# Kernel optimization log

Measured on AMD Instinct MI355X. Metric: run time of the kernel, lower is better.

Reference implementation:

```python
import jax, jax.numpy as jnp
import numpy as np

H, DH, RK, RD = 16, 128, 512, 64  # num_heads, head_dim, kv_lora_rank, rope_dim


def apply_rope(x, cos, sin):
    # x: [..., L, ..., rope_dim]; cos/sin: [L, rope_dim//2]
    cos = cos[None, :, None, :]
    sin = sin[None, :, None, :]
    x1, x2 = x[..., 0::2], x[..., 1::2]
    out_real = x1 * cos - x2 * sin
    out_imag = x1 * sin + x2 * cos
    return jnp.stack([out_real, out_imag], axis=-1).reshape(x.shape)


def setup_inputs() -> dict:
    key = jax.random.key(0)
    ks = jax.random.split(key, 7)
    B, L, E, MAXLEN = 2, 2048, 2048, 4096
    x = jax.random.normal(ks[0], (B, L, E), dtype=jnp.float32)
    cos_table = jax.random.uniform(ks[1], (MAXLEN, RD // 2), dtype=jnp.float32)
    sin_table = jax.random.uniform(ks[2], (MAXLEN, RD // 2), dtype=jnp.float32)
    wq = jax.random.normal(ks[3], (E, H * (DH + RD)), dtype=jnp.float32) / np.sqrt(E)
    wkv_down = jax.random.normal(ks[4], (E, RK + RD), dtype=jnp.float32) / np.sqrt(E)
    w_up = jax.random.normal(ks[5], (RK, H * (2 * DH + RD)), dtype=jnp.float32) / np.sqrt(RK)
    w_out = jax.random.normal(ks[6], (H * (DH + RD), E), dtype=jnp.float32) / np.sqrt(H * (DH + RD))
    return {"x": x, "cos_table": cos_table, "sin_table": sin_table,
            "wq": wq, "wkv_down": wkv_down, "w_up": w_up, "w_out": w_out}


def reference(x, cos_table, sin_table, wq, wkv_down, w_up, w_out):
    # Prefill path (use_cache=False): idx = 0, kv comes from current tokens only.
    B, L, E = x.shape
    cos = cos_table[:L]
    sin = sin_table[:L]

    # Queries: per-head content part + rope part
    q_all = (x @ wq).reshape(B, L, H, DH + RD)
    q_head, q_rope = q_all[..., :DH], q_all[..., DH:]
    q_rope = apply_rope(q_rope, cos, sin)
    q = jnp.concatenate([q_head, q_rope], axis=-1)  # [B,L,H,DH+RD]

    # Compressed KV latent + shared rope key
    kv_lat = x @ wkv_down                            # [B,L,RK+RD]
    c_kv = kv_lat[..., :RK]
    k_rope = kv_lat[..., RK:]
    k_rope = apply_rope(k_rope[:, :, None, :], cos, sin)[:, :, 0, :]  # [B,L,RD]

    # Up-project latent to per-head K/V
    up = (c_kv @ w_up).reshape(B, L, H, 2 * DH + RD)
    k_head = up[..., :DH]
    v_head = up[..., DH:2 * DH]
    v_rope = up[..., 2 * DH:]
    k_rope_b = jnp.broadcast_to(k_rope[:, :, None, :], (B, L, H, RD))
    k = jnp.concatenate([k_head, k_rope_b], axis=-1)  # [B,L,H,DH+RD]
    v = jnp.concatenate([v_head, v_rope], axis=-1)    # [B,L,H,DH+RD]

    # Causal attention (query_indices = arange(L), key_indices = arange(L))
    scale = 1.0 / jnp.sqrt(jnp.float32(DH + RD))
    scores = jnp.einsum('blhd,bshd->bhls', q, k) * scale
    idxs = jnp.arange(L)
    bias = jnp.where(idxs[:, None] >= idxs[None, :], 0.0, -1000000000.0)
    attn = jax.nn.softmax(scores + bias[None, None, :, :], axis=-1)
    out = jnp.einsum('bhls,bshd->blhd', attn, v)  # [B,L,H,DH+RD]
    return out.reshape(B, L, -1) @ w_out
```

## Files before the change

kernel.cpp:

```cpp
#include <hip/hip_runtime.h>
#include <stdint.h>

#define H_ 16
#define DH_ 128
#define RK_ 512
#define RD_ 64
#define B_ 2
#define L_ 2048
#define E_ 2048
#define DQ_ 192
#define NQ_ (H_*DQ_)
#define NKV_ 576
#define NKVP_ 640
#define NUP_ (H_*(2*DH_+RD_))
#define M_ (B_*L_)

typedef unsigned short u16;
typedef __bf16 bf16x8 __attribute__((ext_vector_type(8)));
typedef float floatx4 __attribute__((ext_vector_type(4)));

__device__ __forceinline__ u16 f2bf(float f) {
    union { float f; uint32_t u; } v; v.f = f;
    uint32_t u = v.u;
    u = (u + 0x7fffu + ((u >> 16) & 1u)) >> 16;
    return (u16)u;
}
__device__ __forceinline__ float bf2f(u16 b) {
    union { uint32_t u; float f; } v; v.u = ((uint32_t)b) << 16; return v.f;
}

__device__ __forceinline__ void gld_lds16(const void* g, void* l) {
    __builtin_amdgcn_global_load_lds((__attribute__((address_space(1))) void*)(g),
                                     (__attribute__((address_space(3))) void*)(l),
                                     16, 0, 0);
}

__global__ void convert_bf16(const float* __restrict__ in, u16* __restrict__ out, int n4) {
    int i = blockIdx.x * blockDim.x + threadIdx.x;
    if (i >= n4) return;
    float4 v = ((const float4*)in)[i];
    uint2 o;
    o.x = (uint32_t)f2bf(v.x) | ((uint32_t)f2bf(v.y) << 16);
    o.y = (uint32_t)f2bf(v.z) | ((uint32_t)f2bf(v.w) << 16);
    ((uint2*)out)[i] = o;
}

__global__ void transpose_w(const float* __restrict__ W, u16* __restrict__ Wt,
                            int K, int N, int Npad) {
    __shared__ float tile[32][33];
    int n0 = blockIdx.x * 32, k0 = blockIdx.y * 32;
    int tx = threadIdx.x, ty = threadIdx.y;
    for (int i = 0; i < 4; i++) {
        int k = k0 + ty + i * 8, n = n0 + tx;
        tile[ty + i * 8][tx] = (n < N) ? W[(size_t)k * N + n] : 0.f;
    }
    __syncthreads();
    for (int i = 0; i < 4; i++) {
        int n = n0 + ty + i * 8, k = k0 + tx;
        Wt[(size_t)n * K + k] = f2bf(tile[tx][ty + i * 8]);
    }
}

__global__ __launch_bounds__(256) void gemm_bt(const u16* __restrict__ A,
                                               const u16* __restrict__ Bt,
                                               float* __restrict__ C,
                                               int M, int N, int K) {
    __shared__ __align__(16) u16 As[128 * 32];
    __shared__ __align__(16) u16 Bs[128 * 32];
    const int tid = threadIdx.x;
    const int wave = tid >> 6, lane = tid & 63;
    const int quad = lane >> 4, l16 = lane & 15;
    const int m0 = blockIdx.y * 128, n0 = blockIdx.x * 128;
    const int wm = (wave >> 1) * 64, wn = (wave & 1) * 64;

    floatx4 zero4 = {0.f, 0.f, 0.f, 0.f};
    floatx4 acc[4][4];
    for (int i = 0; i < 4; i++) for (int j = 0; j < 4; j++) acc[i][j] = zero4;

    const u16* Ab = A + (size_t)m0 * K;
    const u16* Bb = Bt + (size_t)n0 * K;

    for (int k0 = 0; k0 < K; k0 += 32) {
        for (int it = 0; it < 2; ++it) {
            int c = it * 256 + tid;
            int row = c >> 2, cr = c & 3;
            gld_lds16(Ab + (size_t)row * K + k0 + cr * 8, As + c * 8);
            gld_lds16(Bb + (size_t)row * K + k0 + cr * 8, Bs + c * 8);
        }
        __syncthreads();
        bf16x8 af[4], bfr[4];
        for (int i = 0; i < 4; i++) af[i]  = *(const bf16x8*)(As + (wm + i * 16 + l16) * 32 + quad * 8);
        for (int j = 0; j < 4; j++) bfr[j] = *(const bf16x8*)(Bs + (wn + j * 16 + l16) * 32 + quad * 8);
        for (int i = 0; i < 4; i++)
            for (int j = 0; j < 4; j++)
                acc[i][j] = __builtin_amdgcn_mfma_f32_16x16x32_bf16(af[i], bfr[j], acc[i][j], 0, 0, 0);
        __syncthreads();
    }
    for (int i = 0; i < 4; i++)
        for (int j = 0; j < 4; j++) {
            int mrow = m0 + wm + i * 16 + quad * 4;
            int ncol = n0 + wn + j * 16 + l16;
            float* Cp = C + (size_t)mrow * N + ncol;
            for (int r = 0; r < 4; r++) Cp[(size_t)r * N] = acc[i][j][r];
        }
}

__global__ void build_q(const float* __restrict__ q_all, const float* __restrict__ cosT,
                        const float* __restrict__ sinT, u16* __restrict__ qb) {
    const float QS = 0.07216878364870323f * 1.4426950408889634f;
    int idx = blockIdx.x * blockDim.x + threadIdx.x;
    if (idx >= M_ * H_ * 96) return;
    int p = idx % 96; int t = idx / 96; int h = t % H_; int row = t / H_;
    int l = row & (L_ - 1); int b = row >> 11;
    const float* src = q_all + (size_t)row * NQ_ + h * DQ_;
    u16* dst = qb + ((size_t)(b * H_ + h) * L_ + l) * DQ_;
    int d = 2 * p;
    float x1 = src[d], x2 = src[d + 1];
    if (d < DH_) { dst[d] = f2bf(x1 * QS); dst[d + 1] = f2bf(x2 * QS); }
    else {
        int i = (d - DH_) >> 1;
        float c = cosT[(size_t)l * 32 + i], s = sinT[(size_t)l * 32 + i];
        dst[d]     = f2bf((x1 * c - x2 * s) * QS);
        dst[d + 1] = f2bf((x1 * s + x2 * c) * QS);
    }
}

__global__ void build_ckv(const float* __restrict__ kv, const float* __restrict__ cosT,
                          const float* __restrict__ sinT, u16* __restrict__ ckv,
                          u16* __restrict__ kropeb) {
    int idx = blockIdx.x * blockDim.x + threadIdx.x;
    if (idx >= M_ * 288) return;
    int j = idx % 288; int row = idx / 288;
    int l = row & (L_ - 1);
    const float* src = kv + (size_t)row * NKVP_;
    if (j < 256) {
        ckv[(size_t)row * RK_ + 2 * j]     = f2bf(src[2 * j]);
        ckv[(size_t)row * RK_ + 2 * j + 1] = f2bf(src[2 * j + 1]);
    } else {
        int i = j - 256;
        float x1 = src[RK_ + 2 * i], x2 = src[RK_ + 2 * i + 1];
        float c = cosT[(size_t)l * 32 + i], s = sinT[(size_t)l * 32 + i];
        kropeb[(size_t)row * RD_ + 2 * i]     = f2bf(x1 * c - x2 * s);
        kropeb[(size_t)row * RD_ + 2 * i + 1] = f2bf(x1 * s + x2 * c);
    }
}

__global__ __launch_bounds__(256) void build_kvt(const float* __restrict__ up,
        const u16* __restrict__ kropeb, u16* __restrict__ kb, u16* __restrict__ vtb) {
    __shared__ float vt[64][193];
    int blk = blockIdx.x;
    int lt = blk & 31; int bh = blk >> 5; int h = bh % H_; int b = bh / H_;
    int tid = threadIdx.x;
    int l0 = lt * 64;
    for (int it = 0; it < 48; ++it) {
        int idx = it * 256 + tid;
        int lr = idx / 192, d = idx % 192;
        size_t row = (size_t)b * L_ + l0 + lr;
        float vv = (d < DH_) ? up[row * NUP_ + h * 320 + DH_ + d]
                             : up[row * NUP_ + h * 320 + 2 * DH_ + (d - DH_)];
        vt[lr][d] = vv;
        u16 kbf = (d < DH_) ? f2bf(up[row * NUP_ + h * 320 + d])
                            : kropeb[row * RD_ + (d - DH_)];
        kb[((size_t)bh * L_ + l0 + lr) * DQ_ + d] = kbf;
    }
    __syncthreads();
    for (int it = 0; it < 48; ++it) {
        int idx = it * 256 + tid;
        int lr = idx & 63, d = idx >> 6;
        int l = l0 + lr;
        int s5 = l & 31;
        int k5 = ((s5 >> 2) & 3) * 8 + ((s5 >> 4) & 1) * 4 + (s5 & 3);
        int lp = (l & ~31) | k5;
        vtb[((size_t)bh * DQ_ + d) * L_ + lp] = f2bf(vt[lr][d]);
    }
}

__global__ __launch_bounds__(512, 2) void attn(const u16* __restrict__ qb,
        const u16* __restrict__ kb, const u16* __restrict__ vtb,
        u16* __restrict__ po0, u16* __restrict__ po1,
        float* __restrict__ pm0, float* __restrict__ pl0,
        float* __restrict__ pm1, float* __restrict__ pl1) {
    __shared__ __align__(16) u16 Ks[6 * 64 * 32];
    __shared__ __align__(16) u16 Vs[2 * 192 * 32];
    int id = blockIdx.x;
    int bh = id & 31, tj = id >> 5;
    int t = tj >> 1, j = tj & 1;
    int tid = threadIdx.x, wave = tid >> 6, lane = tid & 63;
    int quad = lane >> 4, l16 = lane & 15;

    u16* po = j ? po1 : po0;
    float* pm = j ? pm1 : pm0;
    float* pl = j ? pl1 : pl0;

    const u16* kbase0 = kb + (size_t)bh * L_ * DQ_;
    const u16* vbase0 = vtb + (size_t)bh * (size_t)DQ_ * L_;
    floatx4 zero4 = {0.f, 0.f, 0.f, 0.f};

    for (int seg = 0; seg < 2; ++seg) {
        const int QT = seg == 0 ? (7 - t) : t;
        const int st0 = j ? (2 * QT + 2) : 0;
        const int st1 = j ? (4 * QT + 3) : (2 * QT + 1);

        bf16x8 aq[2][6];
        const u16* qbase = qb + ((size_t)bh * L_ + QT * 256 + wave * 16 + l16) * DQ_;
        for (int a = 0; a < 2; a++)
            for (int kk = 0; kk < 6; kk++)
                aq[a][kk] = *(const bf16x8*)(qbase + a * 128 * DQ_ + kk * 32 + quad * 8);

        floatx4 o[2][12];
        for (int a = 0; a < 2; a++) for (int i = 0; i < 12; i++) o[a][i] = zero4;
        float m_i[2] = {-INFINITY, -INFINITY};
        float l_i[2] = {0.f, 0.f};

        for (int st = st0; st <= st1; ++st) {
            const u16* kg = kbase0 + (size_t)st * 64 * DQ_;
            for (int it = 0; it < 3; ++it) {
                int c = it * 512 + tid;
                int kk = c >> 8, cc = c & 255;
                int s = cc >> 2, q4 = cc & 3;
                gld_lds16(kg + (size_t)s * DQ_ + kk * 32 + q4 * 8, Ks + c * 8);
            }
            const u16* vg = vbase0 + st * 64;
            for (int it = 0; it < 3; ++it) {
                int c = it * 512 + tid;
                int g = (c >= 768) ? 1 : 0;
                int cc = c - g * 768;
                int d = cc >> 2, q4 = cc & 3;
                gld_lds16(vg + (size_t)d * L_ + g * 32 + q4 * 8, Vs + c * 8);
            }
            __syncthreads();

            int R0 = QT * 256 + wave * 16 - st * 64;
            int R1 = R0 + 128;
            int smax0 = min(3, (R0 + 15) >> 4);
            int smax1 = min(3, (R1 + 15) >> 4);
            bool live0 = smax0 >= 0, live1 = smax1 >= 0;

            float pv[2][4][4];
            float mxa[2] = {-INFINITY, -INFINITY};
#pragma unroll
            for (int stile = 0; stile < 4; ++stile) {
                if (stile > smax1) {
                    for (int r = 0; r < 4; r++) { pv[0][stile][r] = 0.f; pv[1][stile][r] = 0.f; }
                    continue;
                }
                bool do0 = (stile <= smax0);
                floatx4 s1v = zero4, s0v = zero4;
                for (int kk = 0; kk < 6; kk++) {
                    bf16x8 kf = *(const bf16x8*)(Ks + kk * 2048 + (stile * 16 + l16) * 32 + quad * 8);
                    s1v = __builtin_amdgcn_mfma_f32_16x16x32_bf16(kf, aq[1][kk], s1v, 0, 0, 0);
                    if (do0) s0v = __builtin_amdgcn_mfma_f32_16x16x32_bf16(kf, aq[0][kk], s0v, 0, 0, 0);
                }
                int sb = stile * 16;
                if (sb + 15 > R1) {
                    for (int r = 0; r < 4; r++) {
                        float v = (sb + quad * 4 + r > R1 + l16) ? -1e30f : s1v[r];
                        pv[1][stile][r] = v; mxa[1] = fmaxf(mxa[1], v);
                    }
                } else {
                    for (int r = 0; r < 4; r++) { pv[1][stile][r] = s1v[r]; mxa[1] = fmaxf(mxa[1], s1v[r]); }
                }
                if (do0) {
                    if (sb + 15 > R0) {
                        for (int r = 0; r < 4; r++) {
                            float v = (sb + quad * 4 + r > R0 + l16) ? -1e30f : s0v[r];
                            pv[0][stile][r] = v; mxa[0] = fmaxf(mxa[0], v);
                        }
                    } else {
                        for (int r = 0; r < 4; r++) { pv[0][stile][r] = s0v[r]; mxa[0] = fmaxf(mxa[0], s0v[r]); }
                    }
                } else {
                    for (int r = 0; r < 4; r++) pv[0][stile][r] = 0.f;
                }
            }

            bf16x8 pf[2][2];
            bool lv[2] = {live0, live1};
            int smx[2] = {smax0, smax1};
#pragma unroll
            for (int a = 0; a < 2; a++) {
                if (!lv[a]) continue;
                float mx = mxa[a];
                mx = fmaxf(mx, __shfl_xor(mx, 16));
                mx = fmaxf(mx, __shfl_xor(mx, 32));
                float mn = fmaxf(m_i[a], mx);
                float alpha = exp2f(m_i[a] - mn);
                m_i[a] = mn;
                float rs = 0.f;
#pragma unroll
                for (int stile = 0; stile < 4; ++stile) {
                    if (stile > smx[a]) continue;
                    for (int r = 0; r < 4; r++) {
                        float e = exp2f(pv[a][stile][r] - mn);
                        pv[a][stile][r] = e;
                        rs += e;
                    }
                }
                rs += __shfl_xor(rs, 16);
                rs += __shfl_xor(rs, 32);
                l_i[a] = l_i[a] * alpha + rs;
                if (__any(alpha != 1.0f))
                    for (int i = 0; i < 12; i++) o[a][i] *= alpha;
                for (int g = 0; g < 2; g++) {
                    union { bf16x8 v; u16 s[8]; } u;
                    for (int r = 0; r < 4; r++) {
                        u.s[r]     = f2bf(pv[a][g * 2][r]);
                        u.s[4 + r] = f2bf(pv[a][g * 2 + 1][r]);
                    }
                    pf[a][g] = u.v;
                }
            }

            for (int g = 0; g < 2; g++)
                for (int dtile = 0; dtile < 12; dtile++) {
                    bf16x8 vf = *(const bf16x8*)(Vs + g * 6144 + (dtile * 16 + l16) * 32 + quad * 8);
                    if (live0)
                        o[0][dtile] = __builtin_amdgcn_mfma_f32_16x16x32_bf16(vf, pf[0][g], o[0][dtile], 0, 0, 0);
                    if (live1)
                        o[1][dtile] = __builtin_amdgcn_mfma_f32_16x16x32_bf16(vf, pf[1][g], o[1][dtile], 0, 0, 0);
                }
            __syncthreads();
        }

        int tile = bh * 8 + QT;
        for (int a = 0; a < 2; a++) {
            int q = a * 128 + wave * 16 + l16;
            u16* dst = po + ((size_t)tile * 256 + q) * 192;
            for (int dtile = 0; dtile < 12; dtile++) {
                ushort4 pk;
                pk.x = f2bf(o[a][dtile][0]);
                pk.y = f2bf(o[a][dtile][1]);
                pk.z = f2bf(o[a][dtile][2]);
                pk.w = f2bf(o[a][dtile][3]);
                *(ushort4*)(dst + dtile * 16 + quad * 4) = pk;
            }
            if (quad == 0) {
                pm[(size_t)tile * 256 + q] = m_i[a];
                pl[(size_t)tile * 256 + q] = l_i[a];
            }
        }
        __syncthreads();
    }
}

__global__ void attn_merge(const u16* __restrict__ po0, const u16* __restrict__ po1,
                           const float* __restrict__ pm0, const float* __restrict__ pl0,
                           const float* __restrict__ pm1, const float* __restrict__ pl1,
                           u16* __restrict__ ao) {
    int idx = blockIdx.x * blockDim.x + threadIdx.x;
    int c = idx % 48; int rest = idx / 48;
    int q = rest & 255; int tile = rest >> 8;
    int bh = tile >> 3, QT = tile & 7;
    size_t mi = (size_t)tile * 256 + q;
    float m0 = pm0[mi], m1 = pm1[mi];
    float l0 = pl0[mi], l1 = pl1[mi];
    float m = fmaxf(m0, m1);
    float a0 = exp2f(m0 - m), a1 = exp2f(m1 - m);
    float inv = 1.0f / (l0 * a0 + l1 * a1);
    float s0 = a0 * inv, s1 = a1 * inv;
    ushort4 u0 = *(const ushort4*)(po0 + mi * 192 + c * 4);
    ushort4 u1 = *(const ushort4*)(po1 + mi * 192 + c * 4);
    int b = bh >> 4, h = bh & 15;
    int l = QT * 256 + q;
    u16* dst = ao + (((size_t)(b * L_ + l)) * H_ + h) * DQ_ + c * 4;
    ushort4 pk;
    pk.x = f2bf(bf2f(u0.x) * s0 + bf2f(u1.x) * s1);
    pk.y = f2bf(bf2f(u0.y) * s0 + bf2f(u1.y) * s1);
    pk.z = f2bf(bf2f(u0.z) * s0 + bf2f(u1.z) * s1);
    pk.w = f2bf(bf2f(u0.w) * s0 + bf2f(u1.w) * s1);
    *(ushort4*)dst = pk;
}

extern "C" void kernel_launch(void* const* d_in, const int* in_sizes, int n_in,
                              void* d_out, int out_size, void* d_ws, size_t ws_size,
                              hipStream_t stream) {
    const float* x    = (const float*)d_in[0];
    const float* cosT = (const float*)d_in[1];
    const float* sinT = (const float*)d_in[2];
    const float* wq   = (const float*)d_in[3];
    const float* wkv  = (const float*)d_in[4];
    const float* wup  = (const float*)d_in[5];
    const float* wout = (const float*)d_in[6];
    float* out = (float*)d_out;
    char* ws = (char*)d_ws;

    size_t off = 0;
    auto alloc = [&](size_t b) { size_t r = off; off += (b + 255) & ~(size_t)255; return r; };
    u16* xb     = (u16*)(ws + alloc((size_t)M_ * E_ * 2));
    u16* wqT    = (u16*)(ws + alloc((size_t)NQ_ * E_ * 2));
    u16* wkvT   = (u16*)(ws + alloc((size_t)NKVP_ * E_ * 2));
    u16* wupT   = (u16*)(ws + alloc((size_t)NUP_ * RK_ * 2));
    u16* woutT  = (u16*)(ws + alloc((size_t)E_ * NQ_ * 2));
    u16* qb     = (u16*)(ws + alloc((size_t)B_ * H_ * L_ * DQ_ * 2));
    u16* kb     = (u16*)(ws + alloc((size_t)B_ * H_ * L_ * DQ_ * 2));
    u16* vtb    = (u16*)(ws + alloc((size_t)B_ * H_ * DQ_ * L_ * 2));
    u16* ao     = (u16*)(ws + alloc((size_t)M_ * NQ_ * 2));
    u16* ckv    = (u16*)(ws + alloc((size_t)M_ * RK_ * 2));
    u16* kropeb = (u16*)(ws + alloc((size_t)M_ * RD_ * 2));
    char* scratch = ws + alloc((size_t)M_ * NUP_ * 4);
    float* q_all  = (float*)(scratch);
    float* kv_lat = (float*)(scratch + (size_t)M_ * NQ_ * 4);
    float* up     = (float*)(scratch);
    size_t poSz = (size_t)256 * 256 * 192 * 2;
    u16*   po0 = (u16*)(scratch);
    u16*   po1 = (u16*)(scratch + poSz);
    float* pm0 = (float*)(scratch + 2 * poSz);
    float* pl0 = (float*)(scratch + 2 * poSz + 256 * 256 * 4);
    float* pm1 = (float*)(scratch + 2 * poSz + 2 * 256 * 256 * 4);
    float* pl1 = (float*)(scratch + 2 * poSz + 3 * 256 * 256 * 4);

    dim3 tb(32, 8);
    int n4 = M_ * E_ / 4;
    convert_bf16<<<(n4 + 255) / 256, 256, 0, stream>>>(x, xb, n4);
    transpose_w<<<dim3(NQ_ / 32, E_ / 32), tb, 0, stream>>>(wq, wqT, E_, NQ_, NQ_);
    transpose_w<<<dim3(NKVP_ / 32, E_ / 32), tb, 0, stream>>>(wkv, wkvT, E_, NKV_, NKVP_);
    transpose_w<<<dim3(NUP_ / 32, RK_ / 32), tb, 0, stream>>>(wup, wupT, RK_, NUP_, NUP_);
    transpose_w<<<dim3(E_ / 32, NQ_ / 32), tb, 0, stream>>>(wout, woutT, NQ_, E_, E_);

    gemm_bt<<<dim3(NQ_ / 128, M_ / 128), 256, 0, stream>>>(xb, wqT, q_all, M_, NQ_, E_);
    gemm_bt<<<dim3(NKVP_ / 128, M_ / 128), 256, 0, stream>>>(xb, wkvT, kv_lat, M_, NKVP_, E_);

    int nq = M_ * H_ * 96;
    build_q<<<(nq + 255) / 256, 256, 0, stream>>>(q_all, cosT, sinT, qb);
    int nc = M_ * 288;
    build_ckv<<<(nc + 255) / 256, 256, 0, stream>>>(kv_lat, cosT, sinT, ckv, kropeb);

    gemm_bt<<<dim3(NUP_ / 128, M_ / 128), 256, 0, stream>>>(ckv, wupT, up, M_, NUP_, RK_);
    build_kvt<<<B_ * H_ * 32, 256, 0, stream>>>(up, kropeb, kb, vtb);

    attn<<<256, 512, 0, stream>>>(qb, kb, vtb, po0, po1, pm0, pl0, pm1, pl1);
    attn_merge<<<(256 * 256 * 48) / 256, 256, 0, stream>>>(po0, po1, pm0, pl0, pm1, pl1, ao);

    gemm_bt<<<dim3(E_ / 128, M_ / 128), 256, 0, stream>>>(ao, woutT, out, M_, E_, NQ_);
}
```

Baseline: 614.5 us.

## Split causal attention KV range into four partitions and merge four partials

The attention kernel now splits each query tile's causal key range into four equal chunks instead of two, and launches 512 blocks instead of 256 so more blocks are resident across the CUs. Partial outputs, maxima and sums for the four chunks go to a larger scratch area, with the first partial reusing the start of the workspace that held the bf16 input and transposed weights. A new merge kernel combines the four partials with log-sum-exp rescaling. This trades doubled partial-result traffic and a heavier merge for better parallelism and balance in the attention phase.

```diff
diff --git a/kernel.cpp b/kernel.cpp
--- a/kernel.cpp
+++ b/kernel.cpp
@@ -177,20 +177,21 @@
 
 __global__ __launch_bounds__(512, 2) void attn(const u16* __restrict__ qb,
         const u16* __restrict__ kb, const u16* __restrict__ vtb,
-        u16* __restrict__ po0, u16* __restrict__ po1,
-        float* __restrict__ pm0, float* __restrict__ pl0,
-        float* __restrict__ pm1, float* __restrict__ pl1) {
+        u16* __restrict__ poX, u16* __restrict__ poB,
+        float* __restrict__ pmB, float* __restrict__ plB) {
     __shared__ __align__(16) u16 Ks[6 * 64 * 32];
     __shared__ __align__(16) u16 Vs[2 * 192 * 32];
     int id = blockIdx.x;
-    int bh = id & 31, tj = id >> 5;
-    int t = tj >> 1, j = tj & 1;
+    int bh = id & 31, rest = id >> 5;
+    int t = rest & 3, j = rest >> 2;
     int tid = threadIdx.x, wave = tid >> 6, lane = tid & 63;
     int quad = lane >> 4, l16 = lane & 15;
 
-    u16* po = j ? po1 : po0;
-    float* pm = j ? pm1 : pm0;
-    float* pl = j ? pl1 : pl0;
+    const size_t poElems = (size_t)256 * 256 * 192;
+    const size_t mlElems = (size_t)256 * 256;
+    u16* po = (j == 0) ? poX : (poB + (size_t)(j - 1) * poElems);
+    float* pm = pmB + (size_t)j * mlElems;
+    float* pl = plB + (size_t)j * mlElems;
 
     const u16* kbase0 = kb + (size_t)bh * L_ * DQ_;
     const u16* vbase0 = vtb + (size_t)bh * (size_t)DQ_ * L_;
@@ -198,8 +199,8 @@
 
     for (int seg = 0; seg < 2; ++seg) {
         const int QT = seg == 0 ? (7 - t) : t;
-        const int st0 = j ? (2 * QT + 2) : 0;
-        const int st1 = j ? (4 * QT + 3) : (2 * QT + 1);
+        const int st0 = j * (QT + 1);
+        const int st1 = st0 + QT;
 
         bf16x8 aq[2][6];
         const u16* qbase = qb + ((size_t)bh * L_ + QT * 256 + wave * 16 + l16) * DQ_;
@@ -343,31 +344,48 @@
     }
 }
 
-__global__ void attn_merge(const u16* __restrict__ po0, const u16* __restrict__ po1,
-                           const float* __restrict__ pm0, const float* __restrict__ pl0,
-                           const float* __restrict__ pm1, const float* __restrict__ pl1,
-                           u16* __restrict__ ao) {
+__global__ void attn_merge4(const u16* __restrict__ poX, const u16* __restrict__ poB,
+                            const float* __restrict__ pmB, const float* __restrict__ plB,
+                            u16* __restrict__ ao) {
+    const size_t poElems = (size_t)256 * 256 * 192;
+    const size_t mlElems = (size_t)256 * 256;
     int idx = blockIdx.x * blockDim.x + threadIdx.x;
     int c = idx % 48; int rest = idx / 48;
     int q = rest & 255; int tile = rest >> 8;
     int bh = tile >> 3, QT = tile & 7;
     size_t mi = (size_t)tile * 256 + q;
-    float m0 = pm0[mi], m1 = pm1[mi];
-    float l0 = pl0[mi], l1 = pl1[mi];
-    float m = fmaxf(m0, m1);
-    float a0 = exp2f(m0 - m), a1 = exp2f(m1 - m);
-    float inv = 1.0f / (l0 * a0 + l1 * a1);
-    float s0 = a0 * inv, s1 = a1 * inv;
-    ushort4 u0 = *(const ushort4*)(po0 + mi * 192 + c * 4);
-    ushort4 u1 = *(const ushort4*)(po1 + mi * 192 + c * 4);
+    float mv[4], lv[4];
+    float m = -INFINITY;
+    for (int jj = 0; jj < 4; jj++) {
+        mv[jj] = pmB[jj * mlElems + mi];
+        lv[jj] = plB[jj * mlElems + mi];
+        m = fmaxf(m, mv[jj]);
+    }
+    float denom = 0.f, sc[4];
+    for (int jj = 0; jj < 4; jj++) {
+        sc[jj] = exp2f(mv[jj] - m);
+        denom += lv[jj] * sc[jj];
+    }
+    float inv = 1.0f / denom;
+    float acc[4] = {0.f, 0.f, 0.f, 0.f};
+    for (int jj = 0; jj < 4; jj++) {
+        float s = sc[jj] * inv;
+        const u16* src = (jj == 0) ? (poX + mi * 192 + c * 4)
+                                   : (poB + (size_t)(jj - 1) * poElems + mi * 192 + c * 4);
+        ushort4 u = *(const ushort4*)src;
+        acc[0] += bf2f(u.x) * s;
+        acc[1] += bf2f(u.y) * s;
+        acc[2] += bf2f(u.z) * s;
+        acc[3] += bf2f(u.w) * s;
+    }
     int b = bh >> 4, h = bh & 15;
     int l = QT * 256 + q;
     u16* dst = ao + (((size_t)(b * L_ + l)) * H_ + h) * DQ_ + c * 4;
     ushort4 pk;
-    pk.x = f2bf(bf2f(u0.x) * s0 + bf2f(u1.x) * s1);
-    pk.y = f2bf(bf2f(u0.y) * s0 + bf2f(u1.y) * s1);
-    pk.z = f2bf(bf2f(u0.z) * s0 + bf2f(u1.z) * s1);
-    pk.w = f2bf(bf2f(u0.w) * s0 + bf2f(u1.w) * s1);
+    pk.x = f2bf(acc[0]);
+    pk.y = f2bf(acc[1]);
+    pk.z = f2bf(acc[2]);
+    pk.w = f2bf(acc[3]);
     *(ushort4*)dst = pk;
 }
 
@@ -401,13 +419,13 @@
     float* q_all  = (float*)(scratch);
     float* kv_lat = (float*)(scratch + (size_t)M_ * NQ_ * 4);
     float* up     = (float*)(scratch);
+
     size_t poSz = (size_t)256 * 256 * 192 * 2;
-    u16*   po0 = (u16*)(scratch);
-    u16*   po1 = (u16*)(scratch + poSz);
-    float* pm0 = (float*)(scratch + 2 * poSz);
-    float* pl0 = (float*)(scratch + 2 * poSz + 256 * 256 * 4);
-    float* pm1 = (float*)(scratch + 2 * poSz + 2 * 256 * 256 * 4);
-    float* pl1 = (float*)(scratch + 2 * poSz + 3 * 256 * 256 * 4);
+    size_t mlSz = (size_t)256 * 256 * 4;
+    u16*   poX = (u16*)(ws);
+    u16*   poB = (u16*)(scratch);
+    float* pmA = (float*)(scratch + 3 * poSz);
+    float* plA = (float*)(scratch + 3 * poSz + 4 * mlSz);
 
     dim3 tb(32, 8);
     int n4 = M_ * E_ / 4;
@@ -428,8 +446,8 @@
     gemm_bt<<<dim3(NUP_ / 128, M_ / 128), 256, 0, stream>>>(ckv, wupT, up, M_, NUP_, RK_);
     build_kvt<<<B_ * H_ * 32, 256, 0, stream>>>(up, kropeb, kb, vtb);
 
-    attn<<<256, 512, 0, stream>>>(qb, kb, vtb, po0, po1, pm0, pl0, pm1, pl1);
-    attn_merge<<<(256 * 256 * 48) / 256, 256, 0, stream>>>(po0, po1, pm0, pl0, pm1, pl1, ao);
+    attn<<<512, 512, 0, stream>>>(qb, kb, vtb, poX, poB, pmA, plA);
+    attn_merge4<<<(256 * 256 * 48) / 256, 256, 0, stream>>>(poX, poB, pmA, plA, ao);
 
     gemm_bt<<<dim3(E_ / 128, M_ / 128), 256, 0, stream>>>(ao, woutT, out, M_, E_, NQ_);
 }
```

Result: slower. 643.8 us (+4.8%).

## Split attention into 128-row query tiles across 512 four-wave blocks

Applied to the files above, without the earlier changes.

The causal attention kernel moves from 256 blocks of 8 waves, each handling 256-row query tiles, to 512 blocks of 4 waves, each handling 128-row query tiles. The KV range per tile is split in two halves (j=0 and j=1), and tiles p and 15-p are paired per block to balance causal work. The merge kernel and the partial-output buffers are resized to match, and one partial buffer now reuses the front of the workspace. The aim is more blocks in flight and better load balance across CUs. In exchange, each K/V tile loaded into LDS is reused by fewer query rows, and the merge pass processes more partial rows.

```diff
diff --git a/kernel.cpp b/kernel.cpp
--- a/kernel.cpp
+++ b/kernel.cpp
@@ -175,37 +175,37 @@
     }
 }
 
-__global__ __launch_bounds__(512, 2) void attn(const u16* __restrict__ qb,
+__global__ __launch_bounds__(256, 2) void attn(const u16* __restrict__ qb,
         const u16* __restrict__ kb, const u16* __restrict__ vtb,
-        u16* __restrict__ po0, u16* __restrict__ po1,
-        float* __restrict__ pm0, float* __restrict__ pl0,
-        float* __restrict__ pm1, float* __restrict__ pl1) {
+        u16* __restrict__ poX, u16* __restrict__ poB,
+        float* __restrict__ pmB, float* __restrict__ plB) {
     __shared__ __align__(16) u16 Ks[6 * 64 * 32];
     __shared__ __align__(16) u16 Vs[2 * 192 * 32];
     int id = blockIdx.x;
-    int bh = id & 31, tj = id >> 5;
-    int t = tj >> 1, j = tj & 1;
+    int bh = id & 31, rest = id >> 5;
+    int p = rest & 7, j = rest >> 3;
     int tid = threadIdx.x, wave = tid >> 6, lane = tid & 63;
     int quad = lane >> 4, l16 = lane & 15;
 
-    u16* po = j ? po1 : po0;
-    float* pm = j ? pm1 : pm0;
-    float* pl = j ? pl1 : pl0;
+    const size_t mlElems = (size_t)512 * 128;
+    u16* po = j ? poB : poX;
+    float* pm = pmB + (size_t)j * mlElems;
+    float* pl = plB + (size_t)j * mlElems;
 
     const u16* kbase0 = kb + (size_t)bh * L_ * DQ_;
     const u16* vbase0 = vtb + (size_t)bh * (size_t)DQ_ * L_;
     floatx4 zero4 = {0.f, 0.f, 0.f, 0.f};
 
     for (int seg = 0; seg < 2; ++seg) {
-        const int QT = seg == 0 ? (7 - t) : t;
-        const int st0 = j ? (2 * QT + 2) : 0;
-        const int st1 = j ? (4 * QT + 3) : (2 * QT + 1);
+        const int QT = seg == 0 ? (15 - p) : p;
+        const int st0 = j * (QT + 1);
+        const int st1 = st0 + QT;
 
         bf16x8 aq[2][6];
-        const u16* qbase = qb + ((size_t)bh * L_ + QT * 256 + wave * 16 + l16) * DQ_;
+        const u16* qbase = qb + ((size_t)bh * L_ + QT * 128 + wave * 16 + l16) * DQ_;
         for (int a = 0; a < 2; a++)
             for (int kk = 0; kk < 6; kk++)
-                aq[a][kk] = *(const bf16x8*)(qbase + a * 128 * DQ_ + kk * 32 + quad * 8);
+                aq[a][kk] = *(const bf16x8*)(qbase + a * 64 * DQ_ + kk * 32 + quad * 8);
 
         floatx4 o[2][12];
         for (int a = 0; a < 2; a++) for (int i = 0; i < 12; i++) o[a][i] = zero4;
@@ -214,15 +214,15 @@
 
         for (int st = st0; st <= st1; ++st) {
             const u16* kg = kbase0 + (size_t)st * 64 * DQ_;
-            for (int it = 0; it < 3; ++it) {
-                int c = it * 512 + tid;
+            for (int it = 0; it < 6; ++it) {
+                int c = it * 256 + tid;
                 int kk = c >> 8, cc = c & 255;
                 int s = cc >> 2, q4 = cc & 3;
                 gld_lds16(kg + (size_t)s * DQ_ + kk * 32 + q4 * 8, Ks + c * 8);
             }
             const u16* vg = vbase0 + st * 64;
-            for (int it = 0; it < 3; ++it) {
-                int c = it * 512 + tid;
+            for (int it = 0; it < 6; ++it) {
+                int c = it * 256 + tid;
                 int g = (c >= 768) ? 1 : 0;
                 int cc = c - g * 768;
                 int d = cc >> 2, q4 = cc & 3;
@@ -230,8 +230,8 @@
             }
             __syncthreads();
 
-            int R0 = QT * 256 + wave * 16 - st * 64;
-            int R1 = R0 + 128;
+            int R0 = QT * 128 + wave * 16 - st * 64;
+            int R1 = R0 + 64;
             int smax0 = min(3, (R0 + 15) >> 4);
             int smax1 = min(3, (R1 + 15) >> 4);
             bool live0 = smax0 >= 0, live1 = smax1 >= 0;
@@ -322,10 +322,10 @@
             __syncthreads();
         }
 
-        int tile = bh * 8 + QT;
+        int tile = bh * 16 + QT;
         for (int a = 0; a < 2; a++) {
-            int q = a * 128 + wave * 16 + l16;
-            u16* dst = po + ((size_t)tile * 256 + q) * 192;
+            int q = a * 64 + wave * 16 + l16;
+            u16* dst = po + ((size_t)tile * 128 + q) * 192;
             for (int dtile = 0; dtile < 12; dtile++) {
                 ushort4 pk;
                 pk.x = f2bf(o[a][dtile][0]);
@@ -335,33 +335,33 @@
                 *(ushort4*)(dst + dtile * 16 + quad * 4) = pk;
             }
             if (quad == 0) {
-                pm[(size_t)tile * 256 + q] = m_i[a];
-                pl[(size_t)tile * 256 + q] = l_i[a];
+                pm[(size_t)tile * 128 + q] = m_i[a];
+                pl[(size_t)tile * 128 + q] = l_i[a];
             }
         }
         __syncthreads();
     }
 }
 
-__global__ void attn_merge(const u16* __restrict__ po0, const u16* __restrict__ po1,
-                           const float* __restrict__ pm0, const float* __restrict__ pl0,
-                           const float* __restrict__ pm1, const float* __restrict__ pl1,
-                           u16* __restrict__ ao) {
+__global__ void attn_merge2(const u16* __restrict__ poX, const u16* __restrict__ poB,
+                            const float* __restrict__ pmB, const float* __restrict__ plB,
+                            u16* __restrict__ ao) {
+    const size_t mlElems = (size_t)512 * 128;
     int idx = blockIdx.x * blockDim.x + threadIdx.x;
     int c = idx % 48; int rest = idx / 48;
-    int q = rest & 255; int tile = rest >> 8;
-    int bh = tile >> 3, QT = tile & 7;
-    size_t mi = (size_t)tile * 256 + q;
-    float m0 = pm0[mi], m1 = pm1[mi];
-    float l0 = pl0[mi], l1 = pl1[mi];
+    int q = rest & 127; int tile = rest >> 7;
+    int bh = tile >> 4, QT = tile & 15;
+    size_t mi = (size_t)tile * 128 + q;
+    float m0 = pmB[mi], m1 = pmB[mlElems + mi];
+    float l0 = plB[mi], l1 = plB[mlElems + mi];
     float m = fmaxf(m0, m1);
     float a0 = exp2f(m0 - m), a1 = exp2f(m1 - m);
     float inv = 1.0f / (l0 * a0 + l1 * a1);
     float s0 = a0 * inv, s1 = a1 * inv;
-    ushort4 u0 = *(const ushort4*)(po0 + mi * 192 + c * 4);
-    ushort4 u1 = *(const ushort4*)(po1 + mi * 192 + c * 4);
+    ushort4 u0 = *(const ushort4*)(poX + mi * 192 + c * 4);
+    ushort4 u1 = *(const ushort4*)(poB + mi * 192 + c * 4);
     int b = bh >> 4, h = bh & 15;
-    int l = QT * 256 + q;
+    int l = QT * 128 + q;
     u16* dst = ao + (((size_t)(b * L_ + l)) * H_ + h) * DQ_ + c * 4;
     ushort4 pk;
     pk.x = f2bf(bf2f(u0.x) * s0 + bf2f(u1.x) * s1);
@@ -401,13 +401,13 @@
     float* q_all  = (float*)(scratch);
     float* kv_lat = (float*)(scratch + (size_t)M_ * NQ_ * 4);
     float* up     = (float*)(scratch);
-    size_t poSz = (size_t)256 * 256 * 192 * 2;
-    u16*   po0 = (u16*)(scratch);
-    u16*   po1 = (u16*)(scratch + poSz);
-    float* pm0 = (float*)(scratch + 2 * poSz);
-    float* pl0 = (float*)(scratch + 2 * poSz + 256 * 256 * 4);
-    float* pm1 = (float*)(scratch + 2 * poSz + 2 * 256 * 256 * 4);
-    float* pl1 = (float*)(scratch + 2 * poSz + 3 * 256 * 256 * 4);
+
+    size_t poSz = (size_t)512 * 128 * 192 * 2;
+    size_t mlSz = (size_t)512 * 128 * 4;
+    u16*   poX = (u16*)(ws);
+    u16*   poB = (u16*)(scratch);
+    float* pmA = (float*)(scratch + poSz);
+    float* plA = (float*)(scratch + poSz + 2 * mlSz);
 
     dim3 tb(32, 8);
     int n4 = M_ * E_ / 4;
@@ -428,8 +428,8 @@
     gemm_bt<<<dim3(NUP_ / 128, M_ / 128), 256, 0, stream>>>(ckv, wupT, up, M_, NUP_, RK_);
     build_kvt<<<B_ * H_ * 32, 256, 0, stream>>>(up, kropeb, kb, vtb);
 
-    attn<<<256, 512, 0, stream>>>(qb, kb, vtb, po0, po1, pm0, pl0, pm1, pl1);
-    attn_merge<<<(256 * 256 * 48) / 256, 256, 0, stream>>>(po0, po1, pm0, pl0, pm1, pl1, ao);
+    attn<<<512, 256, 0, stream>>>(qb, kb, vtb, poX, poB, pmA, plA);
+    attn_merge2<<<(512 * 128 * 48) / 256, 256, 0, stream>>>(poX, poB, pmA, plA, ao);
 
     gemm_bt<<<dim3(E_ / 128, M_ / 128), 256, 0, stream>>>(ao, woutT, out, M_, E_, NQ_);
 }
```

After: 620.4 us. Within noise of the previous version (+1.0%).
